# Kernel optimization log

Measured on AMD Instinct MI355X. Metric: run time of the kernel, lower is better.

Reference implementation:

```python
import jax, jax.numpy as jnp
import numpy as np

MUL = 32            # multiplicity of 0e and 1o irreps
IN_DIM = MUL * 4    # 32 scalars + 32 vectors = 128
SH_DIM = 4          # 1x0e + 1x1o
N_EDGE_FEAT = 128
HIDDEN = 128
W_NUMEL = 4 * MUL * MUL  # 4 CG paths, uvw weights 32x1x32 each
EPS = 1e-5
INV_SQRT3 = 1.0 / np.sqrt(3.0)
PATH_NORM = 1.0 / np.sqrt(2.0 * MUL)  # 2 paths per output irrep, fan-in MUL


def _fc(edge_attr, W1, b1, W2, b2):
    h = jax.nn.relu(edge_attr @ W1 + b1)
    return h @ W2 + b2  # [E, W_NUMEL]


def _tensor_product(x, sh, w):
    # FullyConnectedTensorProduct for (32x0e+32x1o) x (1x0e+1x1o) -> (32x0e+32x1o)
    # CG (real w3j): 0x0->0: 1 ; 0x1->1, 1x0->1, 1x1->0: delta/sqrt(3)
    E = x.shape[0]
    x0 = x[:, :MUL]                      # [E,32]   scalars
    x1 = x[:, MUL:].reshape(E, MUL, 3)   # [E,32,3] vectors
    sh0 = sh[:, 0]                       # [E]
    sh1 = sh[:, 1:4]                     # [E,3]
    wA = w[:, 0 * MUL * MUL:1 * MUL * MUL].reshape(E, MUL, MUL)  # 0e x 0e -> 0e
    wB = w[:, 1 * MUL * MUL:2 * MUL * MUL].reshape(E, MUL, MUL)  # 0e x 1o -> 1o
    wC = w[:, 2 * MUL * MUL:3 * MUL * MUL].reshape(E, MUL, MUL)  # 1o x 0e -> 1o
    wD = w[:, 3 * MUL * MUL:4 * MUL * MUL].reshape(E, MUL, MUL)  # 1o x 1o -> 0e
    out0 = PATH_NORM * (
        jnp.einsum('eu,euw->ew', x0 * sh0[:, None], wA)
        + INV_SQRT3 * jnp.einsum('eui,ei,euw->ew', x1, sh1, wD))
    out1 = PATH_NORM * INV_SQRT3 * (
        jnp.einsum('eu,ei,euw->ewi', x0, sh1, wB)
        + jnp.einsum('eui,euw->ewi', x1 * sh0[:, None, None], wC))
    return jnp.concatenate([out0, out1.reshape(E, MUL * 3)], axis=-1)  # [E,128]


def _batch_norm(x, bn_weight, bn_bias):
    # e3nn-style equivariant BatchNorm (training stats): scalars get mean/var
    # normalization + affine; vectors get norm normalization + scale.
    N = x.shape[0]
    s = x[:, :MUL]                       # [N,32]
    v = x[:, MUL:].reshape(N, MUL, 3)    # [N,32,3]
    s = s - s.mean(axis=0)
    s = s * (jax.lax.rsqrt((s ** 2).mean(axis=0) + EPS) * bn_weight[:MUL]) + bn_bias
    v_norm = jax.lax.rsqrt((v ** 2).mean(axis=-1).mean(axis=0) + EPS)  # [32]
    v = v * (v_norm * bn_weight[MUL:])[None, :, None]
    return jnp.concatenate([s, v.reshape(N, MUL * 3)], axis=-1)


def _forward(node_attr, edge_index, edge_attr, edge_sh,
             W1, b1, W2, b2, bn_weight, bn_bias):
    edge_src, edge_dst = edge_index[0], edge_index[1]
    N = node_attr.shape[0]
    w = _fc(edge_attr, W1, b1, W2, b2)                     # [E, 4096]
    tp = _tensor_product(node_attr[edge_dst], edge_sh, w)  # [E, 128]
    # scatter mean over edge_src
    summed = jax.ops.segment_sum(tp, edge_src, num_segments=N)
    counts = jax.ops.segment_sum(jnp.ones((tp.shape[0],), tp.dtype), edge_src,
                                 num_segments=N)
    out = summed / jnp.maximum(counts, 1.0)[:, None]
    out = out + node_attr                                  # residual (same dim, pad=0)
    return _batch_norm(out, bn_weight, bn_bias)


def setup_inputs() -> dict:
    key = jax.random.key(0)
    ks = jax.random.split(key, 10)
    N, E = 10000, 60000
    node_attr = jax.random.normal(ks[0], (N, IN_DIM), jnp.float32)
    edge_index = jax.random.randint(ks[1], (2, E), 0, N)
    edge_attr = jax.random.normal(ks[2], (E, N_EDGE_FEAT), jnp.float32)
    edge_sh = jax.random.normal(ks[3], (E, SH_DIM), jnp.float32)
    W1 = jax.random.normal(ks[4], (N_EDGE_FEAT, HIDDEN), jnp.float32) / np.sqrt(N_EDGE_FEAT)
    b1 = jnp.zeros((HIDDEN,), jnp.float32)
    W2 = jax.random.normal(ks[5], (HIDDEN, W_NUMEL), jnp.float32) / np.sqrt(HIDDEN)
    b2 = jnp.zeros((W_NUMEL,), jnp.float32)
    bn_weight = jnp.ones((2 * MUL,), jnp.float32)
    bn_bias = jnp.zeros((MUL,), jnp.float32)
    return {"node_attr": node_attr, "edge_index": edge_index,
            "edge_attr": edge_attr, "edge_sh": edge_sh,
            "W1": W1, "b1": b1, "W2": W2, "b2": b2,
            "bn_weight": bn_weight, "bn_bias": bn_bias}


def reference(node_attr, edge_index, edge_attr, edge_sh,
              W1, b1, W2, b2, bn_weight, bn_bias):
    return _forward(node_attr, edge_index, edge_attr, edge_sh,
                    W1, b1, W2, b2, bn_weight, bn_bias)
```

## Files before the change

kernel.cpp:

```cpp
#include <hip/hip_runtime.h>
#include <math.h>

#define EPSV 1e-5f
#define IS3  0.57735026918962576f
#define PNRM 0.125f

typedef __attribute__((ext_vector_type(8)))  short  short8;
typedef __attribute__((ext_vector_type(16))) float  floatx16;

static __device__ inline unsigned short f2bf(float f) {
    unsigned int u = __float_as_uint(f);
    return (unsigned short)((u + 0x7fff + ((u >> 16) & 1)) >> 16);
}
static __device__ inline float bflo(unsigned int u) { return __uint_as_float(u << 16); }
static __device__ inline float bfhi(unsigned int u) { return __uint_as_float(u & 0xffff0000u); }

#define GLD16(gp, lp) __builtin_amdgcn_global_load_lds( \
    (const __attribute__((address_space(1))) unsigned int*)(gp), \
    (__attribute__((address_space(3))) unsigned int*)(lp), 16, 0, 0)

__global__ __launch_bounds__(256) void k0_tile(const float* __restrict__ W2,
                                               const float* __restrict__ W1,
                                               unsigned short* __restrict__ W2T,
                                               unsigned short* __restrict__ W1T,
                                               int* __restrict__ zbase, int zn) {
    const int bx = blockIdx.x, tid = threadIdx.x;
    if (bx >= 132) {
        int i = (bx - 132) * 256 + tid;
        if (i < zn) zbase[i] = 0;
        return;
    }
    __shared__ float tile[128 * 33];
    const float* src;
    unsigned short* dst;
    int nc, tb;
    if (bx < 128) { src = W2; dst = W2T; nc = 4096; tb = bx; }
    else          { src = W1; dst = W1T; nc = 128;  tb = bx - 128; }
    const int c0 = tb * 32;
#pragma unroll
    for (int r = 0; r < 16; ++r) {
        int lin = r * 256 + tid;
        int k = lin >> 5, c = lin & 31;
        tile[k * 33 + c] = src[(size_t)k * nc + c0 + c];
    }
    __syncthreads();
#pragma unroll
    for (int r = 0; r < 2; ++r) {
        int g = r * 256 + tid;
        int kc = g >> 5, c = g & 31;
        short8 v;
#pragma unroll
        for (int j = 0; j < 8; ++j)
            v[j] = (short)f2bf(tile[(kc * 8 + j) * 33 + c]);
        *(short8*)(dst + (size_t)tb * 4096 + kc * 256 + c * 8) = v;
    }
}

__global__ __launch_bounds__(256) void k1_fc(const float* __restrict__ ea,
                                             const unsigned short* __restrict__ W1T,
                                             const float* __restrict__ b1,
                                             const int* __restrict__ ei,
                                             unsigned short* __restrict__ hsw,
                                             int* __restrict__ deg, int E) {
    __shared__ __align__(16) unsigned short W1s[16384];
    __shared__ __align__(16) unsigned short bounce[4 * 1056];
    const int tid = threadIdx.x, lane = tid & 63, wv = tid >> 6;
    const int half = lane >> 5, col = lane & 31;
    const int e0 = blockIdx.x * 128;

    if (tid < 128) { int e = e0 + tid; if (e < E) atomicAdd(&deg[ei[e]], 1); }

#pragma unroll
    for (int q = 0; q < 8; ++q) {
        int chunk = wv * 8 + q;
        GLD16((const char*)W1T + chunk * 1024 + lane * 16, (char*)W1s + chunk * 1024);
    }

    int e = e0 + wv * 32 + col; if (e >= E) e = E - 1;
    short8 afr[8];
#pragma unroll
    for (int c = 0; c < 8; ++c) {
        const float4* p = (const float4*)(ea + (size_t)e * 128 + c * 16 + half * 8);
        float4 f0 = p[0], f1 = p[1];
        short8 v;
        v[0] = (short)f2bf(f0.x); v[1] = (short)f2bf(f0.y);
        v[2] = (short)f2bf(f0.z); v[3] = (short)f2bf(f0.w);
        v[4] = (short)f2bf(f1.x); v[5] = (short)f2bf(f1.y);
        v[6] = (short)f2bf(f1.z); v[7] = (short)f2bf(f1.w);
        afr[c] = v;
    }
    __syncthreads();

    unsigned short* myb = bounce + wv * 1056;
    const int gg = blockIdx.x * 4 + wv;
#pragma unroll
    for (int jt = 0; jt < 4; ++jt) {
        floatx16 d = {0,0,0,0,0,0,0,0,0,0,0,0,0,0,0,0};
#pragma unroll
        for (int c = 0; c < 8; ++c) {
            short8 bf = *(const short8*)((const char*)W1s + jt * 8192 + (2 * c + half) * 512 + col * 16);
            d = __builtin_amdgcn_mfma_f32_32x32x16_bf16(afr[c], bf, d, 0, 0, 0);
        }
        float b1v = b1[jt * 32 + col];
#pragma unroll
        for (int reg = 0; reg < 16; ++reg) {
            int r = (reg & 3) + 8 * (reg >> 2) + 4 * half;
            float v = d[reg] + b1v;
            v = v > 0.f ? v : 0.f;
            myb[(col >> 3) * 264 + r * 8 + (col & 7)] = f2bf(v);
        }
#pragma unroll
        for (int s = 0; s < 2; ++s) {
            short8 v = *(const short8*)&myb[(s * 2 + (lane >> 5)) * 264 + (lane & 31) * 8];
            *(short8*)(hsw + (size_t)gg * 4096 + jt * 1024 + s * 512 + lane * 8) = v;
        }
    }
}

__global__ __launch_bounds__(256, 2) void k2_mfma(const unsigned short* __restrict__ hsw,
                                                  const unsigned short* __restrict__ W2T,
                                                  const float* __restrict__ b2,
                                                  const float* __restrict__ na,
                                                  const int* __restrict__ ei,
                                                  const float* __restrict__ sh,
                                                  const int* __restrict__ rowptr,
                                                  int* __restrict__ cursor,
                                                  int* __restrict__ elist,
                                                  float* __restrict__ tp, int E) {
    __shared__ __align__(16) char smem[32768];
    unsigned short* Ctb = (unsigned short*)smem;
    float* red = (float*)smem;

    const int tid = threadIdx.x, lane = tid & 63, wv = tid >> 6;
    const int half = lane >> 5, col = lane & 31;
    const int ust = wv >> 1, esub = wv & 1;
    const int e0 = blockIdx.x * 64;

    if (tid < 64) {
        int e = e0 + tid;
        if (e < E) {
            int s = ei[e];
            int pos = rowptr[s] + atomicAdd(&cursor[s], 1);
            elist[pos] = e;
        }
    }

    for (int idx = tid; idx < 2048; idx += 256) {
        int el = idx & 63, u = idx >> 6;
        int e = e0 + el; int ec = e < E ? e : E - 1;
        int dn = ei[E + ec];
        const float* nar = na + (size_t)dn * 128;
        float x0  = nar[u];
        float x10 = nar[32 + u * 3], x11 = nar[33 + u * 3], x12 = nar[34 + u * 3];
        const float* shr = sh + (size_t)ec * 4;
        float s0 = shr[0], s1 = shr[1], s2 = shr[2], s3 = shr[3];
        int o = u * 64 + el;
        Ctb[0 * 2048 + o] = f2bf(PNRM * x0 * s0);
        Ctb[1 * 2048 + o] = f2bf(PNRM * IS3 * x0);
        Ctb[2 * 2048 + o] = f2bf(PNRM * IS3 * s0 * x10);
        Ctb[3 * 2048 + o] = f2bf(PNRM * IS3 * s0 * x11);
        Ctb[4 * 2048 + o] = f2bf(PNRM * IS3 * s0 * x12);
        Ctb[5 * 2048 + o] = f2bf(PNRM * IS3 * (x10 * s1 + x11 * s2 + x12 * s3));
    }

    const int gg = blockIdx.x * 2 + esub;
    short8 afr[8];
#pragma unroll
    for (int c = 0; c < 8; ++c)
        afr[c] = *(const short8*)(hsw + (size_t)gg * 4096 + (2 * c + half) * 256 + col * 8);

    __syncthreads();

    float acc0[16] = {}, accB[16] = {}, accC0[16] = {}, accC1[16] = {}, accC2[16] = {};
    const int elb0 = esub * 32 + half * 4;
    const unsigned short* bbase = W2T + half * 256 + col * 8;

#define LOADB(p, br, b2r) do {                                         \
        int _ct = 2 * (p) + ust;                                       \
        const unsigned short* _bp = bbase + (size_t)_ct * 4096;        \
        _Pragma("unroll")                                              \
        for (int _c = 0; _c < 8; ++_c)                                 \
            (br)[_c] = *(const short8*)(_bp + _c * 512);               \
        (b2r) = b2[_ct * 32 + col];                                    \
    } while (0)

#define COMPUTE(p, br, b2v) do {                                                              \
        const int _ct = 2 * (p) + ust;                                                        \
        const int _b = _ct >> 5, _u = _ct & 31;                                               \
        floatx16 d = {0,0,0,0,0,0,0,0,0,0,0,0,0,0,0,0};                                       \
        _Pragma("unroll")                                                                     \
        for (int _c = 0; _c < 8; ++_c)                                                        \
            d = __builtin_amdgcn_mfma_f32_32x32x16_bf16(afr[_c], (br)[_c], d, 0, 0, 0);       \
        if (_b == 0 || _b == 3) {                                                             \
            const unsigned short* tb = Ctb + (_b == 0 ? 0 : 5) * 2048;                        \
            _Pragma("unroll")                                                                 \
            for (int q = 0; q < 4; ++q) {                                                     \
                uint2 cv = *(const uint2*)&tb[_u * 64 + elb0 + q * 8];                        \
                acc0[q * 4 + 0] += bflo(cv.x) * (d[q * 4 + 0] + (b2v));                       \
                acc0[q * 4 + 1] += bfhi(cv.x) * (d[q * 4 + 1] + (b2v));                       \
                acc0[q * 4 + 2] += bflo(cv.y) * (d[q * 4 + 2] + (b2v));                       \
                acc0[q * 4 + 3] += bfhi(cv.y) * (d[q * 4 + 3] + (b2v));                       \
            }                                                                                 \
        } else if (_b == 1) {                                                                 \
            _Pragma("unroll")                                                                 \
            for (int q = 0; q < 4; ++q) {                                                     \
                uint2 cv = *(const uint2*)&Ctb[1 * 2048 + _u * 64 + elb0 + q * 8];            \
                accB[q * 4 + 0] += bflo(cv.x) * (d[q * 4 + 0] + (b2v));                       \
                accB[q * 4 + 1] += bfhi(cv.x) * (d[q * 4 + 1] + (b2v));                       \
                accB[q * 4 + 2] += bflo(cv.y) * (d[q * 4 + 2] + (b2v));                       \
                accB[q * 4 + 3] += bfhi(cv.y) * (d[q * 4 + 3] + (b2v));                       \
            }                                                                                 \
        } else {                                                                              \
            _Pragma("unroll")                                                                 \
            for (int q = 0; q < 4; ++q) {                                                     \
                uint2 cu0 = *(const uint2*)&Ctb[2 * 2048 + _u * 64 + elb0 + q * 8];           \
                uint2 cu1 = *(const uint2*)&Ctb[3 * 2048 + _u * 64 + elb0 + q * 8];           \
                uint2 cu2 = *(const uint2*)&Ctb[4 * 2048 + _u * 64 + elb0 + q * 8];           \
                float f0[4] = {bflo(cu0.x), bfhi(cu0.x), bflo(cu0.y), bfhi(cu0.y)};           \
                float f1[4] = {bflo(cu1.x), bfhi(cu1.x), bflo(cu1.y), bfhi(cu1.y)};           \
                float f2[4] = {bflo(cu2.x), bfhi(cu2.x), bflo(cu2.y), bfhi(cu2.y)};           \
                _Pragma("unroll")                                                             \
                for (int rr = 0; rr < 4; ++rr) {                                              \
                    float v = d[q * 4 + rr] + (b2v);                                          \
                    accC0[q * 4 + rr] += f0[rr] * v;                                          \
                    accC1[q * 4 + rr] += f1[rr] * v;                                          \
                    accC2[q * 4 + rr] += f2[rr] * v;                                          \
                }                                                                             \
            }                                                                                 \
        }                                                                                     \
    } while (0)

    short8 bA[8], bB[8], bC[8];
    float b2A, b2B, b2C;
    LOADB(0, bA, b2A); LOADB(1, bB, b2B); LOADB(2, bC, b2C);
    for (int p = 0; p < 60; p += 3) {
        COMPUTE(p,     bA, b2A); LOADB(p + 3, bA, b2A);
        COMPUTE(p + 1, bB, b2B); LOADB(p + 4, bB, b2B);
        COMPUTE(p + 2, bC, b2C); LOADB(p + 5, bC, b2C);
    }
    COMPUTE(60, bA, b2A); LOADB(63, bA, b2A);
    COMPUTE(61, bB, b2B);
    COMPUTE(62, bC, b2C);
    COMPUTE(63, bA, b2A);
#undef LOADB
#undef COMPUTE

    __syncthreads();
    if (ust == 1) {
#pragma unroll
        for (int q = 0; q < 4; ++q) {
#pragma unroll
            for (int rr = 0; rr < 4; ++rr) {
                int reg = q * 4 + rr;
                int el = esub * 32 + q * 8 + half * 4 + rr;
                int e = e0 + el; int ec = e < E ? e : E - 1;
                float4 sv = *(const float4*)(sh + (size_t)ec * 4);
                red[(((esub * 4 + 0) * 16 + reg) << 6) + lane] = acc0[reg];
                red[(((esub * 4 + 1) * 16 + reg) << 6) + lane] = sv.y * accB[reg] + accC0[reg];
                red[(((esub * 4 + 2) * 16 + reg) << 6) + lane] = sv.z * accB[reg] + accC1[reg];
                red[(((esub * 4 + 3) * 16 + reg) << 6) + lane] = sv.w * accB[reg] + accC2[reg];
            }
        }
    }
    __syncthreads();
    if (ust == 0) {
#pragma unroll
        for (int q = 0; q < 4; ++q) {
#pragma unroll
            for (int rr = 0; rr < 4; ++rr) {
                int reg = q * 4 + rr;
                int el = esub * 32 + q * 8 + half * 4 + rr;
                int e = e0 + el;
                if (e >= E) continue;
                float4 sv = *(const float4*)(sh + (size_t)e * 4);
                float a0 = acc0[reg] + red[(((esub * 4 + 0) * 16 + reg) << 6) + lane];
                float o0 = sv.y * accB[reg] + accC0[reg] + red[(((esub * 4 + 1) * 16 + reg) << 6) + lane];
                float o1 = sv.z * accB[reg] + accC1[reg] + red[(((esub * 4 + 2) * 16 + reg) << 6) + lane];
                float o2 = sv.w * accB[reg] + accC2[reg] + red[(((esub * 4 + 3) * 16 + reg) << 6) + lane];
                float* tpe = tp + (size_t)e * 128;
                tpe[col] = a0;
                tpe[32 + col * 3 + 0] = o0;
                tpe[32 + col * 3 + 1] = o1;
                tpe[32 + col * 3 + 2] = o2;
            }
        }
    }
}

__global__ __launch_bounds__(1024) void k_scan(const int* __restrict__ deg,
                                               int* __restrict__ rowptr, int N) {
    __shared__ int part[1024];
    const int tid = threadIdx.x;
    const int chunk = (N + 1023) / 1024;
    const int base = tid * chunk;
    int s = 0;
    for (int i = 0; i < chunk; ++i) {
        int n = base + i;
        if (n < N) s += deg[n];
    }
    part[tid] = s;
    __syncthreads();
    for (int off = 1; off < 1024; off <<= 1) {
        int t = 0;
        if (tid >= off) t = part[tid - off];
        __syncthreads();
        if (tid >= off) part[tid] += t;
        __syncthreads();
    }
    int prefix = (tid == 0) ? 0 : part[tid - 1];
    for (int i = 0; i < chunk; ++i) {
        int n = base + i;
        if (n < N) { rowptr[n] = prefix; prefix += deg[n]; }
    }
    if (tid == 0) rowptr[N] = part[1023];
}

__global__ __launch_bounds__(256) void k4_gather(const float* __restrict__ tp,
                                                 const int* __restrict__ rowptr,
                                                 const int* __restrict__ elist,
                                                 const float* __restrict__ na,
                                                 float* __restrict__ pre,
                                                 float* __restrict__ stats, int N) {
    __shared__ float bns[96];
    const int tid = threadIdx.x;
    if (tid < 96) bns[tid] = 0.f;
    __syncthreads();
    const int o = tid & 127, hf = tid >> 7;
    for (int n = blockIdx.x * 2 + hf; n < N; n += gridDim.x * 2) {
        int r0 = rowptr[n], r1 = rowptr[n + 1];
        float s = 0.f;
        for (int j = r0; j < r1; ++j)
            s += tp[(size_t)elist[j] * 128 + o];
        int dg = r1 - r0;
        float cf = (float)(dg > 0 ? dg : 1);
        float v = s / cf + na[(size_t)n * 128 + o];
        pre[(size_t)n * 128 + o] = v;
        if (o < 32) {
            atomicAdd(&bns[o], v);
            atomicAdd(&bns[32 + o], v * v);
        } else {
            atomicAdd(&bns[64 + (o - 32) / 3], v * v);
        }
    }
    __syncthreads();
    if (tid < 96) atomicAdd(&stats[tid], bns[tid]);
}

__global__ __launch_bounds__(256) void k5_bn(const float* __restrict__ pre,
                                             const float* __restrict__ stats,
                                             const float* __restrict__ bnw,
                                             const float* __restrict__ bnb,
                                             float* __restrict__ out, int N) {
    size_t idx = (size_t)blockIdx.x * 256 + threadIdx.x;
    if (idx >= (size_t)N * 128) return;
    int o = (int)(idx & 127);
    float v = pre[idx];
    float invN = 1.f / (float)N;
    if (o < 32) {
        float m   = stats[o] * invN;
        float var = stats[32 + o] * invN - m * m;
        out[idx] = (v - m) * rsqrtf(var + EPSV) * bnw[o] + bnb[o];
    } else {
        int j = (o - 32) / 3;
        float vn = rsqrtf(stats[64 + j] * invN * (1.f / 3.f) + EPSV);
        out[idx] = v * vn * bnw[32 + j];
    }
}

extern "C" void kernel_launch(void* const* d_in, const int* in_sizes, int n_in,
                              void* d_out, int out_size, void* d_ws, size_t ws_size,
                              hipStream_t stream) {
    const float* node_attr  = (const float*)d_in[0];
    const int*   edge_index = (const int*)d_in[1];
    const float* edge_attr  = (const float*)d_in[2];
    const float* edge_sh    = (const float*)d_in[3];
    const float* W1  = (const float*)d_in[4];
    const float* b1  = (const float*)d_in[5];
    const float* W2  = (const float*)d_in[6];
    const float* b2  = (const float*)d_in[7];
    const float* bnw = (const float*)d_in[8];
    const float* bnb = (const float*)d_in[9];

    const int N = in_sizes[0] / 128;
    const int E = in_sizes[1] / 2;
    const int ngroups = ((E + 127) / 128) * 4;

    float* tp     = (float*)d_ws;
    float* pre    = tp + (size_t)E * 128;
    float* stats  = pre + (size_t)N * 128;
    int*   deg    = (int*)(stats + 96);
    int*   cursor = deg + N;
    int*   rowptr = cursor + N;
    int*   elist  = rowptr + N + 1;
    char* pbase = (char*)(elist + E);
    pbase += (16 - ((size_t)pbase & 15)) & 15;
    unsigned short* hsw = (unsigned short*)pbase;
    unsigned short* W2T = hsw + (size_t)ngroups * 4096;
    unsigned short* W1T = W2T + (size_t)524288;

    const int zn = 96 + 2 * N;
    const int zblocks = (zn + 255) / 256;

    k0_tile<<<132 + zblocks, 256, 0, stream>>>(W2, W1, W2T, W1T, (int*)stats, zn);
    k1_fc<<<(E + 127) / 128, 256, 0, stream>>>(edge_attr, W1T, b1, edge_index, hsw, deg, E);
    k_scan<<<1, 1024, 0, stream>>>(deg, rowptr, N);
    k2_mfma<<<(E + 63) / 64, 256, 0, stream>>>(hsw, W2T, b2, node_attr, edge_index,
                                               edge_sh, rowptr, cursor, elist, tp, E);
    k4_gather<<<1024, 256, 0, stream>>>(tp, rowptr, elist, node_attr, pre, stats, N);
    size_t ntot = (size_t)N * 128;
    k5_bn<<<(int)((ntot + 255) / 256), 256, 0, stream>>>(pre, stats, bnw, bnb,
                                                         (float*)d_out, N);
}
```

Measured before the change: 260.0 us.

## Stage W2T tiles through double-buffered LDS shared by a 128-edge block

```diff
diff --git a/kernel.cpp b/kernel.cpp
--- a/kernel.cpp
+++ b/kernel.cpp
@@ -117,7 +117,7 @@
     }
 }
 
-__global__ __launch_bounds__(256, 2) void k2_mfma(const unsigned short* __restrict__ hsw,
+__global__ __launch_bounds__(512, 2) void k2_mfma(const unsigned short* __restrict__ hsw,
                                                   const unsigned short* __restrict__ W2T,
                                                   const float* __restrict__ b2,
                                                   const float* __restrict__ na,
@@ -127,16 +127,17 @@
                                                   int* __restrict__ cursor,
                                                   int* __restrict__ elist,
                                                   float* __restrict__ tp, int E) {
-    __shared__ __align__(16) char smem[32768];
-    unsigned short* Ctb = (unsigned short*)smem;
+    __shared__ __align__(16) char smem[131072];
+    unsigned short* Ctb = (unsigned short*)(smem + 65536);
+    const float* b2s = (const float*)(smem + 114688);
     float* red = (float*)smem;
 
     const int tid = threadIdx.x, lane = tid & 63, wv = tid >> 6;
     const int half = lane >> 5, col = lane & 31;
-    const int ust = wv >> 1, esub = wv & 1;
-    const int e0 = blockIdx.x * 64;
-
-    if (tid < 64) {
+    const int esub = wv >> 1, ust = wv & 1;
+    const int e0 = blockIdx.x * 128;
+
+    if (tid < 128) {
         int e = e0 + tid;
         if (e < E) {
             int s = ei[e];
@@ -145,8 +146,8 @@
         }
     }
 
-    for (int idx = tid; idx < 2048; idx += 256) {
-        int el = idx & 63, u = idx >> 6;
+    for (int idx = tid; idx < 4096; idx += 512) {
+        int el = idx & 127, u = idx >> 7;
         int e = e0 + el; int ec = e < E ? e : E - 1;
         int dn = ei[E + ec];
         const float* nar = na + (size_t)dn * 128;
@@ -154,74 +155,75 @@
         float x10 = nar[32 + u * 3], x11 = nar[33 + u * 3], x12 = nar[34 + u * 3];
         const float* shr = sh + (size_t)ec * 4;
         float s0 = shr[0], s1 = shr[1], s2 = shr[2], s3 = shr[3];
-        int o = u * 64 + el;
-        Ctb[0 * 2048 + o] = f2bf(PNRM * x0 * s0);
-        Ctb[1 * 2048 + o] = f2bf(PNRM * IS3 * x0);
-        Ctb[2 * 2048 + o] = f2bf(PNRM * IS3 * s0 * x10);
-        Ctb[3 * 2048 + o] = f2bf(PNRM * IS3 * s0 * x11);
-        Ctb[4 * 2048 + o] = f2bf(PNRM * IS3 * s0 * x12);
-        Ctb[5 * 2048 + o] = f2bf(PNRM * IS3 * (x10 * s1 + x11 * s2 + x12 * s3));
-    }
-
-    const int gg = blockIdx.x * 2 + esub;
+        int o = u * 128 + el;
+        Ctb[0 * 4096 + o] = f2bf(PNRM * x0 * s0);
+        Ctb[1 * 4096 + o] = f2bf(PNRM * IS3 * x0);
+        Ctb[2 * 4096 + o] = f2bf(PNRM * IS3 * s0 * x10);
+        Ctb[3 * 4096 + o] = f2bf(PNRM * IS3 * s0 * x11);
+        Ctb[4 * 4096 + o] = f2bf(PNRM * IS3 * s0 * x12);
+        Ctb[5 * 4096 + o] = f2bf(PNRM * IS3 * (x10 * s1 + x11 * s2 + x12 * s3));
+    }
+
+    const int gg = blockIdx.x * 4 + esub;
     short8 afr[8];
 #pragma unroll
     for (int c = 0; c < 8; ++c)
         afr[c] = *(const short8*)(hsw + (size_t)gg * 4096 + (2 * c + half) * 256 + col * 8);
 
-    __syncthreads();
+#pragma unroll
+    for (int r = 0; r < 2; ++r) {
+        int chunk = wv * 2 + r;
+        GLD16((const char*)b2 + chunk * 1024 + lane * 16, smem + 114688 + chunk * 1024);
+    }
+#pragma unroll
+    for (int q = 0; q < 4; ++q) {
+        int chunk = wv * 4 + q;
+        GLD16((const char*)W2T + chunk * 1024 + lane * 16, smem + chunk * 1024);
+    }
 
     float acc0[16] = {}, accB[16] = {}, accC0[16] = {}, accC1[16] = {}, accC2[16] = {};
     const int elb0 = esub * 32 + half * 4;
-    const unsigned short* bbase = W2T + half * 256 + col * 8;
-
-#define LOADB(p, br, b2r) do {                                         \
-        int _ct = 2 * (p) + ust;                                       \
-        const unsigned short* _bp = bbase + (size_t)_ct * 4096;        \
-        _Pragma("unroll")                                              \
-        for (int _c = 0; _c < 8; ++_c)                                 \
-            (br)[_c] = *(const short8*)(_bp + _c * 512);               \
-        (b2r) = b2[_ct * 32 + col];                                    \
-    } while (0)
-
-#define COMPUTE(p, br, b2v) do {                                                              \
-        const int _ct = 2 * (p) + ust;                                                        \
-        const int _b = _ct >> 5, _u = _ct & 31;                                               \
+
+#define COMPUTE_T(ct_, bb_) do {                                                              \
+        const int _b = (ct_) >> 5, _u = (ct_) & 31;                                           \
         floatx16 d = {0,0,0,0,0,0,0,0,0,0,0,0,0,0,0,0};                                       \
         _Pragma("unroll")                                                                     \
-        for (int _c = 0; _c < 8; ++_c)                                                        \
-            d = __builtin_amdgcn_mfma_f32_32x32x16_bf16(afr[_c], (br)[_c], d, 0, 0, 0);       \
+        for (int _c = 0; _c < 8; ++_c) {                                                      \
+            short8 bf = *(const short8*)((bb_) + (2 * _c + half) * 512 + col * 16);           \
+            d = __builtin_amdgcn_mfma_f32_32x32x16_bf16(afr[_c], bf, d, 0, 0, 0);             \
+        }                                                                                     \
+        const float b2v = b2s[(ct_) * 32 + col];                                              \
         if (_b == 0 || _b == 3) {                                                             \
-            const unsigned short* tb = Ctb + (_b == 0 ? 0 : 5) * 2048;                        \
+            const unsigned short* tb = Ctb + (_b == 0 ? 0 : 5) * 4096;                        \
             _Pragma("unroll")                                                                 \
             for (int q = 0; q < 4; ++q) {                                                     \
-                uint2 cv = *(const uint2*)&tb[_u * 64 + elb0 + q * 8];                        \
-                acc0[q * 4 + 0] += bflo(cv.x) * (d[q * 4 + 0] + (b2v));                       \
-                acc0[q * 4 + 1] += bfhi(cv.x) * (d[q * 4 + 1] + (b2v));                       \
-                acc0[q * 4 + 2] += bflo(cv.y) * (d[q * 4 + 2] + (b2v));                       \
-                acc0[q * 4 + 3] += bfhi(cv.y) * (d[q * 4 + 3] + (b2v));                       \
+                uint2 cv = *(const uint2*)&tb[_u * 128 + elb0 + q * 8];                       \
+                acc0[q * 4 + 0] += bflo(cv.x) * (d[q * 4 + 0] + b2v);                         \
+                acc0[q * 4 + 1] += bfhi(cv.x) * (d[q * 4 + 1] + b2v);                         \
+                acc0[q * 4 + 2] += bflo(cv.y) * (d[q * 4 + 2] + b2v);                         \
+                acc0[q * 4 + 3] += bfhi(cv.y) * (d[q * 4 + 3] + b2v);                         \
             }                                                                                 \
         } else if (_b == 1) {                                                                 \
             _Pragma("unroll")                                                                 \
             for (int q = 0; q < 4; ++q) {                                                     \
-                uint2 cv = *(const uint2*)&Ctb[1 * 2048 + _u * 64 + elb0 + q * 8];            \
-                accB[q * 4 + 0] += bflo(cv.x) * (d[q * 4 + 0] + (b2v));                       \
-                accB[q * 4 + 1] += bfhi(cv.x) * (d[q * 4 + 1] + (b2v));                       \
-                accB[q * 4 + 2] += bflo(cv.y) * (d[q * 4 + 2] + (b2v));                       \
-                accB[q * 4 + 3] += bfhi(cv.y) * (d[q * 4 + 3] + (b2v));                       \
+                uint2 cv = *(const uint2*)&Ctb[1 * 4096 + _u * 128 + elb0 + q * 8];           \
+                accB[q * 4 + 0] += bflo(cv.x) * (d[q * 4 + 0] + b2v);                         \
+                accB[q * 4 + 1] += bfhi(cv.x) * (d[q * 4 + 1] + b2v);                         \
+                accB[q * 4 + 2] += bflo(cv.y) * (d[q * 4 + 2] + b2v);                         \
+                accB[q * 4 + 3] += bfhi(cv.y) * (d[q * 4 + 3] + b2v);                         \
             }                                                                                 \
         } else {                                                                              \
             _Pragma("unroll")                                                                 \
             for (int q = 0; q < 4; ++q) {                                                     \
-                uint2 cu0 = *(const uint2*)&Ctb[2 * 2048 + _u * 64 + elb0 + q * 8];           \
-                uint2 cu1 = *(const uint2*)&Ctb[3 * 2048 + _u * 64 + elb0 + q * 8];           \
-                uint2 cu2 = *(const uint2*)&Ctb[4 * 2048 + _u * 64 + elb0 + q * 8];           \
+                uint2 cu0 = *(const uint2*)&Ctb[2 * 4096 + _u * 128 + elb0 + q * 8];          \
+                uint2 cu1 = *(const uint2*)&Ctb[3 * 4096 + _u * 128 + elb0 + q * 8];          \
+                uint2 cu2 = *(const uint2*)&Ctb[4 * 4096 + _u * 128 + elb0 + q * 8];          \
                 float f0[4] = {bflo(cu0.x), bfhi(cu0.x), bflo(cu0.y), bfhi(cu0.y)};           \
                 float f1[4] = {bflo(cu1.x), bfhi(cu1.x), bflo(cu1.y), bfhi(cu1.y)};           \
                 float f2[4] = {bflo(cu2.x), bfhi(cu2.x), bflo(cu2.y), bfhi(cu2.y)};           \
                 _Pragma("unroll")                                                             \
                 for (int rr = 0; rr < 4; ++rr) {                                              \
-                    float v = d[q * 4 + rr] + (b2v);                                          \
+                    float v = d[q * 4 + rr] + b2v;                                            \
                     accC0[q * 4 + rr] += f0[rr] * v;                                          \
                     accC1[q * 4 + rr] += f1[rr] * v;                                          \
                     accC2[q * 4 + rr] += f2[rr] * v;                                          \
@@ -230,20 +232,23 @@
         }                                                                                     \
     } while (0)
 
-    short8 bA[8], bB[8], bC[8];
-    float b2A, b2B, b2C;
-    LOADB(0, bA, b2A); LOADB(1, bB, b2B); LOADB(2, bC, b2C);
-    for (int p = 0; p < 60; p += 3) {
-        COMPUTE(p,     bA, b2A); LOADB(p + 3, bA, b2A);
-        COMPUTE(p + 1, bB, b2B); LOADB(p + 4, bB, b2B);
-        COMPUTE(p + 2, bC, b2C); LOADB(p + 5, bC, b2C);
-    }
-    COMPUTE(60, bA, b2A); LOADB(63, bA, b2A);
-    COMPUTE(61, bB, b2B);
-    COMPUTE(62, bC, b2C);
-    COMPUTE(63, bA, b2A);
-#undef LOADB
-#undef COMPUTE
+    for (int s = 0; s < 32; ++s) {
+        asm volatile("s_waitcnt vmcnt(0) lgkmcnt(0)" ::: "memory");
+        asm volatile("s_barrier" ::: "memory");
+        if (s + 1 < 32) {
+            const char* gsrc = (const char*)W2T + (size_t)(s + 1) * 32768;
+            char* ldst = smem + ((s + 1) & 1) * 32768;
+#pragma unroll
+            for (int q = 0; q < 4; ++q) {
+                int chunk = wv * 4 + q;
+                GLD16(gsrc + chunk * 1024 + lane * 16, ldst + chunk * 1024);
+            }
+        }
+        const char* buf = smem + (s & 1) * 32768;
+        COMPUTE_T(4 * s + ust,     buf + ust * 8192);
+        COMPUTE_T(4 * s + 2 + ust, buf + (2 + ust) * 8192);
+    }
+#undef COMPUTE_T
 
     __syncthreads();
     if (ust == 1) {
@@ -404,8 +409,8 @@
     k0_tile<<<132 + zblocks, 256, 0, stream>>>(W2, W1, W2T, W1T, (int*)stats, zn);
     k1_fc<<<(E + 127) / 128, 256, 0, stream>>>(edge_attr, W1T, b1, edge_index, hsw, deg, E);
     k_scan<<<1, 1024, 0, stream>>>(deg, rowptr, N);
-    k2_mfma<<<(E + 63) / 64, 256, 0, stream>>>(hsw, W2T, b2, node_attr, edge_index,
-                                               edge_sh, rowptr, cursor, elist, tp, E);
+    k2_mfma<<<(E + 127) / 128, 512, 0, stream>>>(hsw, W2T, b2, node_attr, edge_index,
+                                                 edge_sh, rowptr, cursor, elist, tp, E);
     k4_gather<<<1024, 256, 0, stream>>>(tp, rowptr, elist, node_attr, pre, stats, N);
     size_t ntot = (size_t)N * 128;
     k5_bn<<<(int)((ntot + 255) / 256), 256, 0, stream>>>(pre, stats, bnw, bnb,
```

Result: slower. 286.7 us (+10.3%).

## Switch per-edge TP kernel to 16x16x32 MFMA with per-wave 16-edge tiles

Applied to the files above, without the earlier changes.

```diff
diff --git a/kernel.cpp b/kernel.cpp
--- a/kernel.cpp
+++ b/kernel.cpp
@@ -1,4 +1,5 @@
 #include <hip/hip_runtime.h>
+#include <hip/hip_bf16.h>
 #include <math.h>
 
 #define EPSV 1e-5f
@@ -6,11 +7,17 @@
 #define PNRM 0.125f
 
 typedef __attribute__((ext_vector_type(8)))  short  short8;
+typedef __attribute__((ext_vector_type(4)))  float  floatx4;
 typedef __attribute__((ext_vector_type(16))) float  floatx16;
 
 static __device__ inline unsigned short f2bf(float f) {
     unsigned int u = __float_as_uint(f);
     return (unsigned short)((u + 0x7fff + ((u >> 16) & 1)) >> 16);
+}
+static __device__ inline unsigned int f2bf2(float lo, float hi) {
+    union { __hip_bfloat162 b; unsigned int u; } cv;
+    cv.b = __float22bfloat162_rn(make_float2(lo, hi));
+    return cv.u;
 }
 static __device__ inline float bflo(unsigned int u) { return __uint_as_float(u << 16); }
 static __device__ inline float bfhi(unsigned int u) { return __uint_as_float(u & 0xffff0000u); }
@@ -48,11 +55,11 @@
     for (int r = 0; r < 2; ++r) {
         int g = r * 256 + tid;
         int kc = g >> 5, c = g & 31;
-        short8 v;
-#pragma unroll
-        for (int j = 0; j < 8; ++j)
-            v[j] = (short)f2bf(tile[(kc * 8 + j) * 33 + c]);
-        *(short8*)(dst + (size_t)tb * 4096 + kc * 256 + c * 8) = v;
+        union { unsigned int u[4]; short8 s; } v;
+#pragma unroll
+        for (int j = 0; j < 4; ++j)
+            v.u[j] = f2bf2(tile[(kc * 8 + 2 * j) * 33 + c], tile[(kc * 8 + 2 * j + 1) * 33 + c]);
+        *(short8*)(dst + (size_t)tb * 4096 + kc * 256 + c * 8) = v.s;
     }
 }
 
@@ -82,17 +89,15 @@
     for (int c = 0; c < 8; ++c) {
         const float4* p = (const float4*)(ea + (size_t)e * 128 + c * 16 + half * 8);
         float4 f0 = p[0], f1 = p[1];
-        short8 v;
-        v[0] = (short)f2bf(f0.x); v[1] = (short)f2bf(f0.y);
-        v[2] = (short)f2bf(f0.z); v[3] = (short)f2bf(f0.w);
-        v[4] = (short)f2bf(f1.x); v[5] = (short)f2bf(f1.y);
-        v[6] = (short)f2bf(f1.z); v[7] = (short)f2bf(f1.w);
-        afr[c] = v;
+        union { unsigned int u[4]; short8 s; } v;
+        v.u[0] = f2bf2(f0.x, f0.y); v.u[1] = f2bf2(f0.z, f0.w);
+        v.u[2] = f2bf2(f1.x, f1.y); v.u[3] = f2bf2(f1.z, f1.w);
+        afr[c] = v.s;
     }
     __syncthreads();
 
     unsigned short* myb = bounce + wv * 1056;
-    const int gg = blockIdx.x * 4 + wv;
+    const int gbase = blockIdx.x * 8 + wv * 2;
 #pragma unroll
     for (int jt = 0; jt < 4; ++jt) {
         floatx16 d = {0,0,0,0,0,0,0,0,0,0,0,0,0,0,0,0};
@@ -111,13 +116,16 @@
         }
 #pragma unroll
         for (int s = 0; s < 2; ++s) {
-            short8 v = *(const short8*)&myb[(s * 2 + (lane >> 5)) * 264 + (lane & 31) * 8];
-            *(short8*)(hsw + (size_t)gg * 4096 + jt * 1024 + s * 512 + lane * 8) = v;
-        }
-    }
-}
-
-__global__ __launch_bounds__(256, 2) void k2_mfma(const unsigned short* __restrict__ hsw,
+            int lin = s * 64 + lane;
+            int g = lin >> 6, rem = lin & 63;
+            int q = rem >> 4, el = rem & 15;
+            short8 v = *(const short8*)&myb[q * 264 + (g * 16 + el) * 8];
+            *(short8*)(hsw + (size_t)(gbase + g) * 2048 + (jt * 4 + q) * 128 + el * 8) = v;
+        }
+    }
+}
+
+__global__ __launch_bounds__(256, 3) void k2_mfma(const unsigned short* __restrict__ hsw,
                                                   const unsigned short* __restrict__ W2T,
                                                   const float* __restrict__ b2,
                                                   const float* __restrict__ na,
@@ -127,13 +135,10 @@
                                                   int* __restrict__ cursor,
                                                   int* __restrict__ elist,
                                                   float* __restrict__ tp, int E) {
-    __shared__ __align__(16) char smem[32768];
-    unsigned short* Ctb = (unsigned short*)smem;
-    float* red = (float*)smem;
+    __shared__ __align__(16) unsigned short Ctb[8 * 2048];
 
     const int tid = threadIdx.x, lane = tid & 63, wv = tid >> 6;
-    const int half = lane >> 5, col = lane & 31;
-    const int ust = wv >> 1, esub = wv & 1;
+    const int l15 = lane & 15, quad = lane >> 4;
     const int e0 = blockIdx.x * 64;
 
     if (tid < 64) {
@@ -156,133 +161,100 @@
         float s0 = shr[0], s1 = shr[1], s2 = shr[2], s3 = shr[3];
         int o = u * 64 + el;
         Ctb[0 * 2048 + o] = f2bf(PNRM * x0 * s0);
-        Ctb[1 * 2048 + o] = f2bf(PNRM * IS3 * x0);
-        Ctb[2 * 2048 + o] = f2bf(PNRM * IS3 * s0 * x10);
-        Ctb[3 * 2048 + o] = f2bf(PNRM * IS3 * s0 * x11);
-        Ctb[4 * 2048 + o] = f2bf(PNRM * IS3 * s0 * x12);
-        Ctb[5 * 2048 + o] = f2bf(PNRM * IS3 * (x10 * s1 + x11 * s2 + x12 * s3));
-    }
-
-    const int gg = blockIdx.x * 2 + esub;
-    short8 afr[8];
-#pragma unroll
-    for (int c = 0; c < 8; ++c)
-        afr[c] = *(const short8*)(hsw + (size_t)gg * 4096 + (2 * c + half) * 256 + col * 8);
-
-    __syncthreads();
-
-    float acc0[16] = {}, accB[16] = {}, accC0[16] = {}, accC1[16] = {}, accC2[16] = {};
-    const int elb0 = esub * 32 + half * 4;
-    const unsigned short* bbase = W2T + half * 256 + col * 8;
-
-#define LOADB(p, br, b2r) do {                                         \
-        int _ct = 2 * (p) + ust;                                       \
-        const unsigned short* _bp = bbase + (size_t)_ct * 4096;        \
-        _Pragma("unroll")                                              \
-        for (int _c = 0; _c < 8; ++_c)                                 \
-            (br)[_c] = *(const short8*)(_bp + _c * 512);               \
-        (b2r) = b2[_ct * 32 + col];                                    \
+        Ctb[1 * 2048 + o] = f2bf(PNRM * IS3 * s1 * x0);
+        Ctb[2 * 2048 + o] = f2bf(PNRM * IS3 * s2 * x0);
+        Ctb[3 * 2048 + o] = f2bf(PNRM * IS3 * s3 * x0);
+        Ctb[4 * 2048 + o] = f2bf(PNRM * IS3 * s0 * x10);
+        Ctb[5 * 2048 + o] = f2bf(PNRM * IS3 * s0 * x11);
+        Ctb[6 * 2048 + o] = f2bf(PNRM * IS3 * s0 * x12);
+        Ctb[7 * 2048 + o] = f2bf(PNRM * IS3 * (x10 * s1 + x11 * s2 + x12 * s3));
+    }
+
+    const int g16 = blockIdx.x * 4 + wv;
+    short8 afr[4];
+#pragma unroll
+    for (int kc = 0; kc < 4; ++kc)
+        afr[kc] = *(const short8*)(hsw + (size_t)g16 * 2048 + (kc * 4 + quad) * 128 + l15 * 8);
+
+    __syncthreads();
+
+    float acc0[8] = {}, accT0[8] = {}, accT1[8] = {}, accT2[8] = {};
+    const int elb = wv * 16 + quad * 4;
+    const unsigned short* bbase = W2T + quad * 256 + l15 * 8;
+
+#define LOADB(ct, bf, bv0, bv1) do {                                           \
+        const unsigned short* _bp = bbase + (size_t)(ct) * 4096;               \
+        _Pragma("unroll")                                                      \
+        for (int _kc = 0; _kc < 4; ++_kc) {                                    \
+            (bf)[_kc]     = *(const short8*)(_bp + _kc * 1024);                \
+            (bf)[4 + _kc] = *(const short8*)(_bp + _kc * 1024 + 128);          \
+        }                                                                      \
+        (bv0) = b2[(ct) * 32 + l15];                                           \
+        (bv1) = b2[(ct) * 32 + 16 + l15];                                      \
     } while (0)
 
-#define COMPUTE(p, br, b2v) do {                                                              \
-        const int _ct = 2 * (p) + ust;                                                        \
-        const int _b = _ct >> 5, _u = _ct & 31;                                               \
-        floatx16 d = {0,0,0,0,0,0,0,0,0,0,0,0,0,0,0,0};                                       \
+#define COMPUTE(ct, bf, bv0, bv1) do {                                                        \
+        const int _b = (ct) >> 5, _u = (ct) & 31;                                             \
+        floatx4 d0 = {0,0,0,0}, d1 = {0,0,0,0};                                               \
         _Pragma("unroll")                                                                     \
-        for (int _c = 0; _c < 8; ++_c)                                                        \
-            d = __builtin_amdgcn_mfma_f32_32x32x16_bf16(afr[_c], (br)[_c], d, 0, 0, 0);       \
+        for (int _kc = 0; _kc < 4; ++_kc) {                                                   \
+            d0 = __builtin_amdgcn_mfma_f32_16x16x32_bf16(afr[_kc], (bf)[_kc],     d0, 0,0,0); \
+            d1 = __builtin_amdgcn_mfma_f32_16x16x32_bf16(afr[_kc], (bf)[4 + _kc], d1, 0,0,0); \
+        }                                                                                     \
+        const int _off = _u * 64 + elb;                                                       \
         if (_b == 0 || _b == 3) {                                                             \
-            const unsigned short* tb = Ctb + (_b == 0 ? 0 : 5) * 2048;                        \
+            uint2 cv = *(const uint2*)&Ctb[(_b == 0 ? 0 : 7) * 2048 + _off];                  \
+            float cf[4] = {bflo(cv.x), bfhi(cv.x), bflo(cv.y), bfhi(cv.y)};                   \
             _Pragma("unroll")                                                                 \
-            for (int q = 0; q < 4; ++q) {                                                     \
-                uint2 cv = *(const uint2*)&tb[_u * 64 + elb0 + q * 8];                        \
-                acc0[q * 4 + 0] += bflo(cv.x) * (d[q * 4 + 0] + (b2v));                       \
-                acc0[q * 4 + 1] += bfhi(cv.x) * (d[q * 4 + 1] + (b2v));                       \
-                acc0[q * 4 + 2] += bflo(cv.y) * (d[q * 4 + 2] + (b2v));                       \
-                acc0[q * 4 + 3] += bfhi(cv.y) * (d[q * 4 + 3] + (b2v));                       \
-            }                                                                                 \
-        } else if (_b == 1) {                                                                 \
-            _Pragma("unroll")                                                                 \
-            for (int q = 0; q < 4; ++q) {                                                     \
-                uint2 cv = *(const uint2*)&Ctb[1 * 2048 + _u * 64 + elb0 + q * 8];            \
-                accB[q * 4 + 0] += bflo(cv.x) * (d[q * 4 + 0] + (b2v));                       \
-                accB[q * 4 + 1] += bfhi(cv.x) * (d[q * 4 + 1] + (b2v));                       \
-                accB[q * 4 + 2] += bflo(cv.y) * (d[q * 4 + 2] + (b2v));                       \
-                accB[q * 4 + 3] += bfhi(cv.y) * (d[q * 4 + 3] + (b2v));                       \
+            for (int rr = 0; rr < 4; ++rr) {                                                  \
+                acc0[rr]     += cf[rr] * (d0[rr] + (bv0));                                    \
+                acc0[4 + rr] += cf[rr] * (d1[rr] + (bv1));                                    \
             }                                                                                 \
         } else {                                                                              \
+            const int _tb = (_b == 1) ? 1 : 4;                                                \
+            uint2 c0 = *(const uint2*)&Ctb[(_tb + 0) * 2048 + _off];                          \
+            uint2 c1 = *(const uint2*)&Ctb[(_tb + 1) * 2048 + _off];                          \
+            uint2 c2 = *(const uint2*)&Ctb[(_tb + 2) * 2048 + _off];                          \
+            float f0[4] = {bflo(c0.x), bfhi(c0.x), bflo(c0.y), bfhi(c0.y)};                   \
+            float f1[4] = {bflo(c1.x), bfhi(c1.x), bflo(c1.y), bfhi(c1.y)};                   \
+            float f2[4] = {bflo(c2.x), bfhi(c2.x), bflo(c2.y), bfhi(c2.y)};                   \
             _Pragma("unroll")                                                                 \
-            for (int q = 0; q < 4; ++q) {                                                     \
-                uint2 cu0 = *(const uint2*)&Ctb[2 * 2048 + _u * 64 + elb0 + q * 8];           \
-                uint2 cu1 = *(const uint2*)&Ctb[3 * 2048 + _u * 64 + elb0 + q * 8];           \
-                uint2 cu2 = *(const uint2*)&Ctb[4 * 2048 + _u * 64 + elb0 + q * 8];           \
-                float f0[4] = {bflo(cu0.x), bfhi(cu0.x), bflo(cu0.y), bfhi(cu0.y)};           \
-                float f1[4] = {bflo(cu1.x), bfhi(cu1.x), bflo(cu1.y), bfhi(cu1.y)};           \
-                float f2[4] = {bflo(cu2.x), bfhi(cu2.x), bflo(cu2.y), bfhi(cu2.y)};           \
-                _Pragma("unroll")                                                             \
-                for (int rr = 0; rr < 4; ++rr) {                                              \
-                    float v = d[q * 4 + rr] + (b2v);                                          \
-                    accC0[q * 4 + rr] += f0[rr] * v;                                          \
-                    accC1[q * 4 + rr] += f1[rr] * v;                                          \
-                    accC2[q * 4 + rr] += f2[rr] * v;                                          \
-                }                                                                             \
+            for (int rr = 0; rr < 4; ++rr) {                                                  \
+                float v0 = d0[rr] + (bv0), v1 = d1[rr] + (bv1);                               \
+                accT0[rr] += f0[rr] * v0; accT0[4 + rr] += f0[rr] * v1;                       \
+                accT1[rr] += f1[rr] * v0; accT1[4 + rr] += f1[rr] * v1;                       \
+                accT2[rr] += f2[rr] * v0; accT2[4 + rr] += f2[rr] * v1;                       \
             }                                                                                 \
         }                                                                                     \
     } while (0)
 
-    short8 bA[8], bB[8], bC[8];
-    float b2A, b2B, b2C;
-    LOADB(0, bA, b2A); LOADB(1, bB, b2B); LOADB(2, bC, b2C);
-    for (int p = 0; p < 60; p += 3) {
-        COMPUTE(p,     bA, b2A); LOADB(p + 3, bA, b2A);
-        COMPUTE(p + 1, bB, b2B); LOADB(p + 4, bB, b2B);
-        COMPUTE(p + 2, bC, b2C); LOADB(p + 5, bC, b2C);
-    }
-    COMPUTE(60, bA, b2A); LOADB(63, bA, b2A);
-    COMPUTE(61, bB, b2B);
-    COMPUTE(62, bC, b2C);
-    COMPUTE(63, bA, b2A);
+    short8 bA[8], bB[8];
+    float a0, a1, c0v, c1v;
+    LOADB(0, bA, a0, a1);
+    LOADB(1, bB, c0v, c1v);
+    for (int p = 0; p < 128; p += 2) {
+        COMPUTE(p, bA, a0, a1);
+        if (p + 2 < 128) LOADB(p + 2, bA, a0, a1);
+        COMPUTE(p + 1, bB, c0v, c1v);
+        if (p + 3 < 128) LOADB(p + 3, bB, c0v, c1v);
+        if ((p & 7) == 6) __builtin_amdgcn_s_barrier();
+    }
 #undef LOADB
 #undef COMPUTE
 
-    __syncthreads();
-    if (ust == 1) {
-#pragma unroll
-        for (int q = 0; q < 4; ++q) {
-#pragma unroll
-            for (int rr = 0; rr < 4; ++rr) {
-                int reg = q * 4 + rr;
-                int el = esub * 32 + q * 8 + half * 4 + rr;
-                int e = e0 + el; int ec = e < E ? e : E - 1;
-                float4 sv = *(const float4*)(sh + (size_t)ec * 4);
-                red[(((esub * 4 + 0) * 16 + reg) << 6) + lane] = acc0[reg];
-                red[(((esub * 4 + 1) * 16 + reg) << 6) + lane] = sv.y * accB[reg] + accC0[reg];
-                red[(((esub * 4 + 2) * 16 + reg) << 6) + lane] = sv.z * accB[reg] + accC1[reg];
-                red[(((esub * 4 + 3) * 16 + reg) << 6) + lane] = sv.w * accB[reg] + accC2[reg];
-            }
-        }
-    }
-    __syncthreads();
-    if (ust == 0) {
-#pragma unroll
-        for (int q = 0; q < 4; ++q) {
-#pragma unroll
-            for (int rr = 0; rr < 4; ++rr) {
-                int reg = q * 4 + rr;
-                int el = esub * 32 + q * 8 + half * 4 + rr;
-                int e = e0 + el;
-                if (e >= E) continue;
-                float4 sv = *(const float4*)(sh + (size_t)e * 4);
-                float a0 = acc0[reg] + red[(((esub * 4 + 0) * 16 + reg) << 6) + lane];
-                float o0 = sv.y * accB[reg] + accC0[reg] + red[(((esub * 4 + 1) * 16 + reg) << 6) + lane];
-                float o1 = sv.z * accB[reg] + accC1[reg] + red[(((esub * 4 + 2) * 16 + reg) << 6) + lane];
-                float o2 = sv.w * accB[reg] + accC2[reg] + red[(((esub * 4 + 3) * 16 + reg) << 6) + lane];
-                float* tpe = tp + (size_t)e * 128;
-                tpe[col] = a0;
-                tpe[32 + col * 3 + 0] = o0;
-                tpe[32 + col * 3 + 1] = o1;
-                tpe[32 + col * 3 + 2] = o2;
-            }
+#pragma unroll
+    for (int wt = 0; wt < 2; ++wt) {
+#pragma unroll
+        for (int rr = 0; rr < 4; ++rr) {
+            int e = e0 + elb + rr;
+            if (e >= E) continue;
+            int w = wt * 16 + l15;
+            int reg = wt * 4 + rr;
+            float* tpe = tp + (size_t)e * 128;
+            tpe[w] = acc0[reg];
+            tpe[32 + w * 3 + 0] = accT0[reg];
+            tpe[32 + w * 3 + 1] = accT1[reg];
+            tpe[32 + w * 3 + 2] = accT2[reg];
         }
     }
 }
@@ -328,9 +300,14 @@
     const int o = tid & 127, hf = tid >> 7;
     for (int n = blockIdx.x * 2 + hf; n < N; n += gridDim.x * 2) {
         int r0 = rowptr[n], r1 = rowptr[n + 1];
-        float s = 0.f;
-        for (int j = r0; j < r1; ++j)
-            s += tp[(size_t)elist[j] * 128 + o];
+        float s0 = 0.f, s1 = 0.f;
+        int j = r0;
+        for (; j + 1 < r1; j += 2) {
+            s0 += tp[(size_t)elist[j] * 128 + o];
+            s1 += tp[(size_t)elist[j + 1] * 128 + o];
+        }
+        if (j < r1) s0 += tp[(size_t)elist[j] * 128 + o];
+        float s = s0 + s1;
         int dg = r1 - r0;
         float cf = (float)(dg > 0 ? dg : 1);
         float v = s / cf + na[(size_t)n * 128 + o];
@@ -383,7 +360,7 @@
 
     const int N = in_sizes[0] / 128;
     const int E = in_sizes[1] / 2;
-    const int ngroups = ((E + 127) / 128) * 4;
+    const int ngroups = ((E + 127) / 128) * 8;
 
     float* tp     = (float*)d_ws;
     float* pre    = tp + (size_t)E * 128;
@@ -395,7 +372,7 @@
     char* pbase = (char*)(elist + E);
     pbase += (16 - ((size_t)pbase & 15)) & 15;
     unsigned short* hsw = (unsigned short*)pbase;
-    unsigned short* W2T = hsw + (size_t)ngroups * 4096;
+    unsigned short* W2T = hsw + (size_t)ngroups * 2048;
     unsigned short* W1T = W2T + (size_t)524288;
 
     const int zn = 96 + 2 * N;
```

Measured after the change: 626.5 us. 2.41x slower.
